# Kernel tuning notes

Hardware: AMD Instinct MI355X
Metric: run time of the kernel (lower is better)

The kernel has to match this reference:

```python
import math
import jax, jax.numpy as jnp
import numpy as np

D_MODEL = 1024
D_HIDDEN = 2048
N_EXPERTS = 8
TOP_K = 2
CAPACITY_FACTOR = 1.25


def setup_inputs() -> dict:
    key = jax.random.key(0)
    k0, k1, k2, k3 = jax.random.split(key, 4)
    B, T = 2, 2048
    x = jax.random.normal(k0, (B, T, D_MODEL), dtype=jnp.float32)
    # torch nn.Linear stores weight as [out_features, in_features]
    w_router = jax.random.normal(k1, (N_EXPERTS, D_MODEL), dtype=jnp.float32) * 0.02
    w_gate = jax.random.normal(k2, (D_HIDDEN, D_MODEL), dtype=jnp.float32) * 0.02
    w_down = jax.random.normal(k3, (N_EXPERTS, D_MODEL, D_HIDDEN), dtype=jnp.float32) * 0.02
    return {"x": x, "w_router": w_router, "w_gate": w_gate, "w_down": w_down}


def _moe_forward(x, w_router, w_gate, w_down):
    B, T, D = x.shape
    N = B * T
    xf = x.reshape(N, D)

    # Router (computed in fp32, as in the original)
    logits = xf.astype(jnp.float32) @ w_router.T            # [N, E]
    gates = jax.nn.softmax(logits, axis=-1)                  # [N, E]
    topk_gates, topk_idx = jax.lax.top_k(gates, TOP_K)       # [N, K]

    # expert_mask[n, e] = 1 if expert e is among token n's top-k
    expert_mask = jax.nn.one_hot(topk_idx, N_EXPERTS, dtype=jnp.int32).sum(axis=1)  # [N, E]

    # Capacity masking via cumulative position within each expert's buffer
    capacity = math.ceil(N / N_EXPERTS * CAPACITY_FACTOR)
    position_in_expert = jnp.cumsum(expert_mask, axis=0) - 1
    expert_mask = expert_mask * (position_in_expert < capacity)

    keep = jnp.take_along_axis(expert_mask, topk_idx, axis=1) > 0  # [N, K]
    topk_gates = topk_gates * keep
    topk_gates = topk_gates / (topk_gates.sum(axis=-1, keepdims=True) + 1e-6)

    # Shared up-projection + SiLU (dropout = 0)
    hidden = jax.nn.silu(xf @ w_gate.T)                      # [N, H]

    # combine[n, e] = sum_k topk_gates[n, k] * [topk_idx[n, k] == e]
    combine = (topk_gates[:, :, None]
               * jax.nn.one_hot(topk_idx, N_EXPERTS, dtype=topk_gates.dtype)).sum(axis=1)  # [N, E]

    # Combine: y[n] = sum_e combine[n, e] * (hidden[n] @ w_down[e].T)
    # (dropped tokens have combine weight 0, matching the gated index_add in torch)
    y = jnp.zeros((N, D), dtype=x.dtype)
    for e in range(N_EXPERTS):  # small fixed loop over experts
        y = y + combine[:, e:e + 1] * (hidden @ w_down[e].T)
    return y.reshape(B, T, D)


def reference(x, w_router, w_gate, w_down):
    return _moe_forward(x, w_router, w_gate, w_down)
```

## Files before the change

### kernel.cpp

```cpp
#include <hip/hip_runtime.h>
#include <hip/hip_bf16.h>
#include <math.h>

#define NTOK 4096
#define DMODEL 1024
#define DHID 2048
#define NEXP 8
#define CAP 640

typedef __attribute__((ext_vector_type(8))) short short8;
typedef __attribute__((ext_vector_type(4))) float f32x4;

__device__ inline short f2bf(float f) {
    union { float f; unsigned u; } v; v.f = f;
    unsigned r = v.u + 0x7FFF + ((v.u >> 16) & 1);
    return (short)(r >> 16);
}

__global__ __launch_bounds__(256) void router_kernel(
        const float* __restrict__ x, const float* __restrict__ wr,
        int2* __restrict__ topk_idx, float2* __restrict__ topk_gate)
{
    const int token = blockIdx.x * 4 + (threadIdx.x >> 6);
    const int lane  = threadIdx.x & 63;
    const float* xr = x + (size_t)token * DMODEL + lane * 16;
    float acc[NEXP];
#pragma unroll
    for (int e = 0; e < NEXP; e++) acc[e] = 0.f;
#pragma unroll
    for (int j = 0; j < 4; j++) {
        float4 xv = ((const float4*)xr)[j];
#pragma unroll
        for (int e = 0; e < NEXP; e++) {
            float4 wv = ((const float4*)(wr + e * DMODEL + lane * 16))[j];
            acc[e] += xv.x * wv.x + xv.y * wv.y + xv.z * wv.z + xv.w * wv.w;
        }
    }
#pragma unroll
    for (int off = 32; off >= 1; off >>= 1) {
#pragma unroll
        for (int e = 0; e < NEXP; e++) acc[e] += __shfl_xor(acc[e], off, 64);
    }
    if (lane == 0) {
        float m = acc[0];
#pragma unroll
        for (int e = 1; e < NEXP; e++) m = fmaxf(m, acc[e]);
        float den = 0.f, g[NEXP];
#pragma unroll
        for (int e = 0; e < NEXP; e++) { g[e] = __expf(acc[e] - m); den += g[e]; }
        float inv = 1.f / den;
#pragma unroll
        for (int e = 0; e < NEXP; e++) g[e] *= inv;
        int i0 = 0; float l0 = acc[0];
#pragma unroll
        for (int e = 1; e < NEXP; e++) if (acc[e] > l0) { l0 = acc[e]; i0 = e; }
        int i1 = -1; float l1 = -1e30f;
#pragma unroll
        for (int e = 0; e < NEXP; e++) if (e != i0 && acc[e] > l1) { l1 = acc[e]; i1 = e; }
        topk_idx[token]  = make_int2(i0, i1);
        topk_gate[token] = make_float2(g[i0], g[i1]);
    }
}

__global__ __launch_bounds__(1024) void scan_kernel(
        const int2* __restrict__ topk_idx, const float2* __restrict__ topk_gate,
        int* __restrict__ gtok, float* __restrict__ gw, int* __restrict__ gcnt)
{
    __shared__ unsigned long long sb0[1024], sb1[1024];
    const int th = threadIdx.x;
    int2 idx[4]; float2 gt[4];
#pragma unroll
    for (int j = 0; j < 4; j++) { idx[j] = topk_idx[th * 4 + j]; gt[j] = topk_gate[th * 4 + j]; }
    unsigned long long c0 = 0, c1 = 0;
#pragma unroll
    for (int j = 0; j < 4; j++) {
        int e0 = idx[j].x, e1 = idx[j].y;
        if (e0 < 4) c0 += 1ull << (e0 * 16); else c1 += 1ull << ((e0 - 4) * 16);
        if (e1 < 4) c0 += 1ull << (e1 * 16); else c1 += 1ull << ((e1 - 4) * 16);
    }
    const unsigned long long my0 = c0, my1 = c1;
    sb0[th] = c0; sb1[th] = c1;
    __syncthreads();
    for (int d = 1; d < 1024; d <<= 1) {
        unsigned long long a0 = 0, a1 = 0;
        if (th >= d) { a0 = sb0[th - d]; a1 = sb1[th - d]; }
        __syncthreads();
        c0 += a0; c1 += a1;
        sb0[th] = c0; sb1[th] = c1;
        __syncthreads();
    }
    if (th == 1023) {
#pragma unroll
        for (int e = 0; e < 4; e++) gcnt[e]     = min((int)((c0 >> (e * 16)) & 0xFFFF), CAP);
#pragma unroll
        for (int e = 0; e < 4; e++) gcnt[4 + e] = min((int)((c1 >> (e * 16)) & 0xFFFF), CAP);
    }
    const unsigned long long x0 = c0 - my0, x1 = c1 - my1;
    int base[NEXP];
#pragma unroll
    for (int e = 0; e < 4; e++) base[e]     = (int)((x0 >> (e * 16)) & 0xFFFF);
#pragma unroll
    for (int e = 0; e < 4; e++) base[4 + e] = (int)((x1 >> (e * 16)) & 0xFFFF);
#pragma unroll
    for (int j = 0; j < 4; j++) {
        const int n = th * 4 + j;
        const int e0 = idx[j].x, e1 = idx[j].y;
        const int p0 = base[e0]++;
        const int p1 = base[e1]++;
        const bool k0 = p0 < CAP, k1 = p1 < CAP;
        const float gg0 = k0 ? gt[j].x : 0.f, gg1 = k1 ? gt[j].y : 0.f;
        const float invs = 1.f / (gg0 + gg1 + 1e-6f);
        if (k0) { gtok[e0 * CAP + p0] = n; gw[e0 * CAP + p0] = gg0 * invs; }
        if (k1) { gtok[e1 * CAP + p1] = n; gw[e1 * CAP + p1] = gg1 * invs; }
    }
}

__global__ __launch_bounds__(256) void gemm1_kernel(
        const float* __restrict__ X, const float* __restrict__ WG, short* __restrict__ Hid)
{
    __shared__ short As[128][72];
    __shared__ short Bs[128][72];
    const int t = threadIdx.x;
    const int wave = t >> 6, lane = t & 63;
    const int m0 = blockIdx.y * 128, n0 = blockIdx.x * 128;
    const int wm = (wave >> 1) * 64, wn = (wave & 1) * 64;
    const int lm = lane & 15, lq = lane >> 4, lk = lq * 8;
    const int r0 = t >> 3, c8 = (t & 7) * 8;

    f32x4 acc[4][4];
#pragma unroll
    for (int a = 0; a < 4; a++)
#pragma unroll
        for (int b = 0; b < 4; b++) acc[a][b] = (f32x4)(0.f);

    for (int k0 = 0; k0 < DMODEL; k0 += 64) {
#pragma unroll
        for (int i = 0; i < 4; i++) {
            const int row = r0 + i * 32;
            const float* ga = X + (size_t)(m0 + row) * DMODEL + k0 + c8;
            float4 v0 = ((const float4*)ga)[0];
            float4 v1 = ((const float4*)ga)[1];
            short8 s = { f2bf(v0.x), f2bf(v0.y), f2bf(v0.z), f2bf(v0.w),
                         f2bf(v1.x), f2bf(v1.y), f2bf(v1.z), f2bf(v1.w) };
            *(short8*)&As[row][c8] = s;
            const float* gb = WG + (size_t)(n0 + row) * DMODEL + k0 + c8;
            float4 w0 = ((const float4*)gb)[0];
            float4 w1 = ((const float4*)gb)[1];
            short8 sw = { f2bf(w0.x), f2bf(w0.y), f2bf(w0.z), f2bf(w0.w),
                          f2bf(w1.x), f2bf(w1.y), f2bf(w1.z), f2bf(w1.w) };
            *(short8*)&Bs[row][c8] = sw;
        }
        __syncthreads();
#pragma unroll
        for (int kk = 0; kk < 64; kk += 32) {
            short8 af[4], bf[4];
#pragma unroll
            for (int mi = 0; mi < 4; mi++) af[mi] = *(const short8*)&As[wm + mi * 16 + lm][kk + lk];
#pragma unroll
            for (int ni = 0; ni < 4; ni++) bf[ni] = *(const short8*)&Bs[wn + ni * 16 + lm][kk + lk];
#pragma unroll
            for (int mi = 0; mi < 4; mi++)
#pragma unroll
                for (int ni = 0; ni < 4; ni++)
                    acc[mi][ni] = __builtin_amdgcn_mfma_f32_16x16x32_bf16(af[mi], bf[ni], acc[mi][ni], 0, 0, 0);
        }
        __syncthreads();
    }
#pragma unroll
    for (int mi = 0; mi < 4; mi++)
#pragma unroll
        for (int i = 0; i < 4; i++) {
            const int row = m0 + wm + mi * 16 + lq * 4 + i;
#pragma unroll
            for (int ni = 0; ni < 4; ni++) {
                const int col = n0 + wn + ni * 16 + lm;
                const float v = acc[mi][ni][i];
                const float s = v / (1.f + __expf(-v));
                Hid[(size_t)row * DHID + col] = f2bf(s);
            }
        }
}

__global__ __launch_bounds__(256) void gemm2_kernel(
        const short* __restrict__ Hid, const float* __restrict__ WD,
        const int* __restrict__ gtok, const float* __restrict__ gw,
        const int* __restrict__ gcnt, float* __restrict__ Y)
{
    __shared__ short As[128][72];
    __shared__ short Bs[128][72];
    __shared__ int   tok_s[128];
    __shared__ float w_s[128];
    const int e = blockIdx.z;
    const int cnt = gcnt[e];
    const int m0 = blockIdx.y * 128;
    if (m0 >= cnt) return;
    const int n0 = blockIdx.x * 128;
    const int t = threadIdx.x;
    const int wave = t >> 6, lane = t & 63;
    const int wm = (wave >> 1) * 64, wn = (wave & 1) * 64;
    const int lm = lane & 15, lq = lane >> 4, lk = lq * 8;
    const int r0 = t >> 3, c8 = (t & 7) * 8;
    const float* WDe = WD + (size_t)e * DMODEL * DHID;

    if (t < 128) {
        const int r = m0 + t;
        const bool v = r < cnt;
        tok_s[t] = v ? gtok[e * CAP + r] : 0;
        w_s[t]   = v ? gw[e * CAP + r] : 0.f;
    }
    __syncthreads();

    f32x4 acc[4][4];
#pragma unroll
    for (int a = 0; a < 4; a++)
#pragma unroll
        for (int b = 0; b < 4; b++) acc[a][b] = (f32x4)(0.f);

    const int tokA[4] = { tok_s[r0], tok_s[r0 + 32], tok_s[r0 + 64], tok_s[r0 + 96] };

    for (int k0 = 0; k0 < DHID; k0 += 64) {
#pragma unroll
        for (int i = 0; i < 4; i++) {
            const int row = r0 + i * 32;
            uint4 av = *(const uint4*)(Hid + (size_t)tokA[i] * DHID + k0 + c8);
            *(uint4*)&As[row][c8] = av;
            const float* gb = WDe + (size_t)(n0 + row) * DHID + k0 + c8;
            float4 w0 = ((const float4*)gb)[0];
            float4 w1 = ((const float4*)gb)[1];
            short8 sw = { f2bf(w0.x), f2bf(w0.y), f2bf(w0.z), f2bf(w0.w),
                          f2bf(w1.x), f2bf(w1.y), f2bf(w1.z), f2bf(w1.w) };
            *(short8*)&Bs[row][c8] = sw;
        }
        __syncthreads();
#pragma unroll
        for (int kk = 0; kk < 64; kk += 32) {
            short8 af[4], bf[4];
#pragma unroll
            for (int mi = 0; mi < 4; mi++) af[mi] = *(const short8*)&As[wm + mi * 16 + lm][kk + lk];
#pragma unroll
            for (int ni = 0; ni < 4; ni++) bf[ni] = *(const short8*)&Bs[wn + ni * 16 + lm][kk + lk];
#pragma unroll
            for (int mi = 0; mi < 4; mi++)
#pragma unroll
                for (int ni = 0; ni < 4; ni++)
                    acc[mi][ni] = __builtin_amdgcn_mfma_f32_16x16x32_bf16(af[mi], bf[ni], acc[mi][ni], 0, 0, 0);
        }
        __syncthreads();
    }
#pragma unroll
    for (int mi = 0; mi < 4; mi++)
#pragma unroll
        for (int i = 0; i < 4; i++) {
            const int r = wm + mi * 16 + lq * 4 + i;
            const float wr = w_s[r];
            if (wr > 0.f) {
                const int token = tok_s[r];
#pragma unroll
                for (int ni = 0; ni < 4; ni++) {
                    const int col = n0 + wn + ni * 16 + lm;
                    atomicAdd(&Y[(size_t)token * DMODEL + col], acc[mi][ni][i] * wr);
                }
            }
        }
}

extern "C" void kernel_launch(void* const* d_in, const int* in_sizes, int n_in,
                              void* d_out, int out_size, void* d_ws, size_t ws_size,
                              hipStream_t stream) {
    const float* x  = (const float*)d_in[0];
    const float* wr = (const float*)d_in[1];
    const float* wg = (const float*)d_in[2];
    const float* wd = (const float*)d_in[3];
    float* y = (float*)d_out;

    char* w = (char*)d_ws;
    int2*   topk_idx  = (int2*)w;    w += NTOK * sizeof(int2);
    float2* topk_gate = (float2*)w;  w += NTOK * sizeof(float2);
    int*    gtok      = (int*)w;     w += NEXP * CAP * sizeof(int);
    float*  gw        = (float*)w;   w += NEXP * CAP * sizeof(float);
    int*    gcnt      = (int*)w;     w += 256;
    short*  Hid       = (short*)w;   w += (size_t)NTOK * DHID * sizeof(short);

    hipMemsetAsync(y, 0, (size_t)NTOK * DMODEL * sizeof(float), stream);
    router_kernel<<<NTOK / 4, 256, 0, stream>>>(x, wr, topk_idx, topk_gate);
    scan_kernel<<<1, 1024, 0, stream>>>(topk_idx, topk_gate, gtok, gw, gcnt);
    gemm1_kernel<<<dim3(DHID / 128, NTOK / 128), 256, 0, stream>>>(x, wg, Hid);
    gemm2_kernel<<<dim3(DMODEL / 128, (CAP + 127) / 128, NEXP), 256, 0, stream>>>(Hid, wd, gtok, gw, gcnt, y);
}
```

Baseline: 251.3 us.

## Pre-convert operands to bf16 and stream GEMM tiles with async global-to-LDS loads

```diff
diff --git a/kernel.cpp b/kernel.cpp
--- a/kernel.cpp
+++ b/kernel.cpp
@@ -17,7 +17,68 @@
     return (short)(r >> 16);
 }
 
+__device__ inline void async16(const short* g, short* l) {
+    __builtin_amdgcn_global_load_lds(
+        (const __attribute__((address_space(1))) unsigned*)g,
+        (__attribute__((address_space(3))) unsigned*)l, 16, 0, 0);
+}
+
 __global__ __launch_bounds__(256) void router_kernel(
+        const float* __restrict__ x, const float* __restrict__ wr, short* __restrict__ Xb,
+        int2* __restrict__ topk_idx, float2* __restrict__ topk_gate)
+{
+    const int token = blockIdx.x * 4 + (threadIdx.x >> 6);
+    const int lane  = threadIdx.x & 63;
+    const float* xr = x + (size_t)token * DMODEL + lane * 16;
+    float4 xv[4];
+#pragma unroll
+    for (int j = 0; j < 4; j++) xv[j] = ((const float4*)xr)[j];
+    short8 s0 = { f2bf(xv[0].x), f2bf(xv[0].y), f2bf(xv[0].z), f2bf(xv[0].w),
+                  f2bf(xv[1].x), f2bf(xv[1].y), f2bf(xv[1].z), f2bf(xv[1].w) };
+    short8 s1 = { f2bf(xv[2].x), f2bf(xv[2].y), f2bf(xv[2].z), f2bf(xv[2].w),
+                  f2bf(xv[3].x), f2bf(xv[3].y), f2bf(xv[3].z), f2bf(xv[3].w) };
+    short* xo = Xb + (size_t)token * DMODEL + lane * 16;
+    *(short8*)xo = s0;
+    *(short8*)(xo + 8) = s1;
+
+    float acc[NEXP];
+#pragma unroll
+    for (int e = 0; e < NEXP; e++) acc[e] = 0.f;
+#pragma unroll
+    for (int j = 0; j < 4; j++) {
+#pragma unroll
+        for (int e = 0; e < NEXP; e++) {
+            float4 wv = ((const float4*)(wr + e * DMODEL + lane * 16))[j];
+            acc[e] += xv[j].x * wv.x + xv[j].y * wv.y + xv[j].z * wv.z + xv[j].w * wv.w;
+        }
+    }
+#pragma unroll
+    for (int off = 32; off >= 1; off >>= 1) {
+#pragma unroll
+        for (int e = 0; e < NEXP; e++) acc[e] += __shfl_xor(acc[e], off, 64);
+    }
+    if (lane == 0) {
+        float m = acc[0];
+#pragma unroll
+        for (int e = 1; e < NEXP; e++) m = fmaxf(m, acc[e]);
+        float den = 0.f, g[NEXP];
+#pragma unroll
+        for (int e = 0; e < NEXP; e++) { g[e] = __expf(acc[e] - m); den += g[e]; }
+        float inv = 1.f / den;
+#pragma unroll
+        for (int e = 0; e < NEXP; e++) g[e] *= inv;
+        int i0 = 0; float l0 = acc[0];
+#pragma unroll
+        for (int e = 1; e < NEXP; e++) if (acc[e] > l0) { l0 = acc[e]; i0 = e; }
+        int i1 = -1; float l1 = -1e30f;
+#pragma unroll
+        for (int e = 0; e < NEXP; e++) if (e != i0 && acc[e] > l1) { l1 = acc[e]; i1 = e; }
+        topk_idx[token]  = make_int2(i0, i1);
+        topk_gate[token] = make_float2(g[i0], g[i1]);
+    }
+}
+
+__global__ __launch_bounds__(256) void router_fb_kernel(
         const float* __restrict__ x, const float* __restrict__ wr,
         int2* __restrict__ topk_idx, float2* __restrict__ topk_gate)
 {
@@ -62,12 +123,23 @@
     }
 }
 
+__global__ __launch_bounds__(256) void convert_kernel(
+        const float* __restrict__ src, short* __restrict__ dst)
+{
+    const size_t base = ((size_t)blockIdx.x * 256 + threadIdx.x) * 8;
+    float4 a = ((const float4*)(src + base))[0];
+    float4 b = ((const float4*)(src + base))[1];
+    short8 s = { f2bf(a.x), f2bf(a.y), f2bf(a.z), f2bf(a.w),
+                 f2bf(b.x), f2bf(b.y), f2bf(b.z), f2bf(b.w) };
+    *(short8*)(dst + base) = s;
+}
+
 __global__ __launch_bounds__(1024) void scan_kernel(
         const int2* __restrict__ topk_idx, const float2* __restrict__ topk_gate,
         int* __restrict__ gtok, float* __restrict__ gw, int* __restrict__ gcnt)
 {
-    __shared__ unsigned long long sb0[1024], sb1[1024];
-    const int th = threadIdx.x;
+    __shared__ unsigned long long wt0[16], wt1[16];
+    const int th = threadIdx.x, lane = th & 63, wid = th >> 6;
     int2 idx[4]; float2 gt[4];
 #pragma unroll
     for (int j = 0; j < 4; j++) { idx[j] = topk_idx[th * 4 + j]; gt[j] = topk_gate[th * 4 + j]; }
@@ -79,16 +151,17 @@
         if (e1 < 4) c0 += 1ull << (e1 * 16); else c1 += 1ull << ((e1 - 4) * 16);
     }
     const unsigned long long my0 = c0, my1 = c1;
-    sb0[th] = c0; sb1[th] = c1;
+#pragma unroll
+    for (int d = 1; d < 64; d <<= 1) {
+        unsigned long long t0 = __shfl_up(c0, d, 64);
+        unsigned long long t1 = __shfl_up(c1, d, 64);
+        if (lane >= d) { c0 += t0; c1 += t1; }
+    }
+    if (lane == 63) { wt0[wid] = c0; wt1[wid] = c1; }
     __syncthreads();
-    for (int d = 1; d < 1024; d <<= 1) {
-        unsigned long long a0 = 0, a1 = 0;
-        if (th >= d) { a0 = sb0[th - d]; a1 = sb1[th - d]; }
-        __syncthreads();
-        c0 += a0; c1 += a1;
-        sb0[th] = c0; sb1[th] = c1;
-        __syncthreads();
-    }
+    unsigned long long o0 = 0, o1 = 0;
+    for (int w = 0; w < wid; w++) { o0 += wt0[w]; o1 += wt1[w]; }
+    c0 += o0; c1 += o1;
     if (th == 1023) {
 #pragma unroll
         for (int e = 0; e < 4; e++) gcnt[e]     = min((int)((c0 >> (e * 16)) & 0xFFFF), CAP);
@@ -116,6 +189,149 @@
 }
 
 __global__ __launch_bounds__(256) void gemm1_kernel(
+        const short* __restrict__ Xb, const short* __restrict__ WGb, short* __restrict__ Hid)
+{
+    __shared__ __align__(16) short As[128 * 64];
+    __shared__ __align__(16) short Bs[128 * 64];
+    const int t = threadIdx.x;
+    const int wave = t >> 6, lane = t & 63;
+    const int m0 = blockIdx.y * 128, n0 = blockIdx.x * 128;
+    const int wm = (wave >> 1) * 64, wn = (wave & 1) * 64;
+    const int lm = lane & 15, lq = lane >> 4, lk = lq * 8;
+
+    const short *ga[4], *gb[4];
+    short *la[4], *lb[4];
+#pragma unroll
+    for (int j = 0; j < 4; j++) {
+        const int c = j * 256 + t, r = c >> 3, col = (c & 7) * 8;
+        la[j] = &As[c * 8]; lb[j] = &Bs[c * 8];
+        ga[j] = Xb  + (size_t)(m0 + r) * DMODEL + col;
+        gb[j] = WGb + (size_t)(n0 + r) * DMODEL + col;
+    }
+
+    f32x4 acc[4][4];
+#pragma unroll
+    for (int a = 0; a < 4; a++)
+#pragma unroll
+        for (int b = 0; b < 4; b++) acc[a][b] = (f32x4)(0.f);
+
+    for (int k0 = 0; k0 < DMODEL; k0 += 64) {
+#pragma unroll
+        for (int j = 0; j < 4; j++) { async16(ga[j] + k0, la[j]); async16(gb[j] + k0, lb[j]); }
+        __syncthreads();
+#pragma unroll
+        for (int kk = 0; kk < 64; kk += 32) {
+            short8 af[4], bf[4];
+#pragma unroll
+            for (int mi = 0; mi < 4; mi++) af[mi] = *(const short8*)&As[(wm + mi * 16 + lm) * 64 + kk + lk];
+#pragma unroll
+            for (int ni = 0; ni < 4; ni++) bf[ni] = *(const short8*)&Bs[(wn + ni * 16 + lm) * 64 + kk + lk];
+#pragma unroll
+            for (int mi = 0; mi < 4; mi++)
+#pragma unroll
+                for (int ni = 0; ni < 4; ni++)
+                    acc[mi][ni] = __builtin_amdgcn_mfma_f32_16x16x32_bf16(af[mi], bf[ni], acc[mi][ni], 0, 0, 0);
+        }
+        __syncthreads();
+    }
+#pragma unroll
+    for (int mi = 0; mi < 4; mi++)
+#pragma unroll
+        for (int i = 0; i < 4; i++) {
+            const int row = m0 + wm + mi * 16 + lq * 4 + i;
+#pragma unroll
+            for (int ni = 0; ni < 4; ni++) {
+                const int col = n0 + wn + ni * 16 + lm;
+                const float v = acc[mi][ni][i];
+                const float s = v / (1.f + __expf(-v));
+                Hid[(size_t)row * DHID + col] = f2bf(s);
+            }
+        }
+}
+
+__global__ __launch_bounds__(256) void gemm2_kernel(
+        const short* __restrict__ Hid, const short* __restrict__ WDb,
+        const int* __restrict__ gtok, const float* __restrict__ gw,
+        const int* __restrict__ gcnt, float* __restrict__ Y)
+{
+    __shared__ __align__(16) short As[128 * 64];
+    __shared__ __align__(16) short Bs[128 * 64];
+    __shared__ int   tok_s[128];
+    __shared__ float w_s[128];
+    const int e  = blockIdx.x;
+    const int n0 = blockIdx.y * 128;
+    const int m0 = (blockIdx.z >> 1) * 128;
+    const int ks = blockIdx.z & 1;
+    const int cnt = gcnt[e];
+    if (m0 >= cnt) return;
+    const int t = threadIdx.x;
+    const int wave = t >> 6, lane = t & 63;
+    const int wm = (wave >> 1) * 64, wn = (wave & 1) * 64;
+    const int lm = lane & 15, lq = lane >> 4, lk = lq * 8;
+    const short* WDe = WDb + (size_t)e * DMODEL * DHID;
+
+    if (t < 128) {
+        const int r = m0 + t;
+        const bool v = r < cnt;
+        tok_s[t] = v ? gtok[e * CAP + r] : 0;
+        w_s[t]   = v ? gw[e * CAP + r] : 0.f;
+    }
+    __syncthreads();
+
+    const short *ga[4], *gb[4];
+    short *la[4], *lb[4];
+#pragma unroll
+    for (int j = 0; j < 4; j++) {
+        const int c = j * 256 + t, r = c >> 3, col = (c & 7) * 8;
+        la[j] = &As[c * 8]; lb[j] = &Bs[c * 8];
+        ga[j] = Hid + (size_t)tok_s[r] * DHID + col;
+        gb[j] = WDe + (size_t)(n0 + r) * DHID + col;
+    }
+
+    f32x4 acc[4][4];
+#pragma unroll
+    for (int a = 0; a < 4; a++)
+#pragma unroll
+        for (int b = 0; b < 4; b++) acc[a][b] = (f32x4)(0.f);
+
+    const int kbeg = ks * (DHID / 2), kend = kbeg + DHID / 2;
+    for (int k0 = kbeg; k0 < kend; k0 += 64) {
+#pragma unroll
+        for (int j = 0; j < 4; j++) { async16(ga[j] + k0, la[j]); async16(gb[j] + k0, lb[j]); }
+        __syncthreads();
+#pragma unroll
+        for (int kk = 0; kk < 64; kk += 32) {
+            short8 af[4], bf[4];
+#pragma unroll
+            for (int mi = 0; mi < 4; mi++) af[mi] = *(const short8*)&As[(wm + mi * 16 + lm) * 64 + kk + lk];
+#pragma unroll
+            for (int ni = 0; ni < 4; ni++) bf[ni] = *(const short8*)&Bs[(wn + ni * 16 + lm) * 64 + kk + lk];
+#pragma unroll
+            for (int mi = 0; mi < 4; mi++)
+#pragma unroll
+                for (int ni = 0; ni < 4; ni++)
+                    acc[mi][ni] = __builtin_amdgcn_mfma_f32_16x16x32_bf16(af[mi], bf[ni], acc[mi][ni], 0, 0, 0);
+        }
+        __syncthreads();
+    }
+#pragma unroll
+    for (int mi = 0; mi < 4; mi++)
+#pragma unroll
+        for (int i = 0; i < 4; i++) {
+            const int r = wm + mi * 16 + lq * 4 + i;
+            const float wr = w_s[r];
+            if (wr > 0.f) {
+                const int token = tok_s[r];
+#pragma unroll
+                for (int ni = 0; ni < 4; ni++) {
+                    const int col = n0 + wn + ni * 16 + lm;
+                    atomicAdd(&Y[(size_t)token * DMODEL + col], acc[mi][ni][i] * wr);
+                }
+            }
+        }
+}
+
+__global__ __launch_bounds__(256) void gemm1_fb_kernel(
         const float* __restrict__ X, const float* __restrict__ WG, short* __restrict__ Hid)
 {
     __shared__ short As[128][72];
@@ -181,7 +397,7 @@
         }
 }
 
-__global__ __launch_bounds__(256) void gemm2_kernel(
+__global__ __launch_bounds__(256) void gemm2_fb_kernel(
         const short* __restrict__ Hid, const float* __restrict__ WD,
         const int* __restrict__ gtok, const float* __restrict__ gw,
         const int* __restrict__ gcnt, float* __restrict__ Y)
@@ -280,10 +496,26 @@
     float*  gw        = (float*)w;   w += NEXP * CAP * sizeof(float);
     int*    gcnt      = (int*)w;     w += 256;
     short*  Hid       = (short*)w;   w += (size_t)NTOK * DHID * sizeof(short);
+    short*  Xb        = (short*)w;   w += (size_t)NTOK * DMODEL * sizeof(short);
+    short*  WGb       = (short*)w;   w += (size_t)DHID * DMODEL * sizeof(short);
+    short*  WDb       = (short*)w;   w += (size_t)NEXP * DMODEL * DHID * sizeof(short);
+    const size_t need_full = (size_t)(w - (char*)d_ws);
 
     hipMemsetAsync(y, 0, (size_t)NTOK * DMODEL * sizeof(float), stream);
-    router_kernel<<<NTOK / 4, 256, 0, stream>>>(x, wr, topk_idx, topk_gate);
-    scan_kernel<<<1, 1024, 0, stream>>>(topk_idx, topk_gate, gtok, gw, gcnt);
-    gemm1_kernel<<<dim3(DHID / 128, NTOK / 128), 256, 0, stream>>>(x, wg, Hid);
-    gemm2_kernel<<<dim3(DMODEL / 128, (CAP + 127) / 128, NEXP), 256, 0, stream>>>(Hid, wd, gtok, gw, gcnt, y);
-}
+
+    if (ws_size >= need_full) {
+        router_kernel<<<NTOK / 4, 256, 0, stream>>>(x, wr, Xb, topk_idx, topk_gate);
+        convert_kernel<<<(DHID * DMODEL) / (256 * 8), 256, 0, stream>>>(wg, WGb);
+        convert_kernel<<<(NEXP * DMODEL * DHID) / (256 * 8), 256, 0, stream>>>(wd, WDb);
+        scan_kernel<<<1, 1024, 0, stream>>>(topk_idx, topk_gate, gtok, gw, gcnt);
+        gemm1_kernel<<<dim3(DHID / 128, NTOK / 128), 256, 0, stream>>>(Xb, WGb, Hid);
+        gemm2_kernel<<<dim3(NEXP, DMODEL / 128, 2 * ((CAP + 127) / 128)), 256, 0, stream>>>(
+            Hid, WDb, gtok, gw, gcnt, y);
+    } else {
+        router_fb_kernel<<<NTOK / 4, 256, 0, stream>>>(x, wr, topk_idx, topk_gate);
+        scan_kernel<<<1, 1024, 0, stream>>>(topk_idx, topk_gate, gtok, gw, gcnt);
+        gemm1_fb_kernel<<<dim3(DHID / 128, NTOK / 128), 256, 0, stream>>>(x, wg, Hid);
+        gemm2_fb_kernel<<<dim3(DMODEL / 128, (CAP + 127) / 128, NEXP), 256, 0, stream>>>(
+            Hid, wd, gtok, gw, gcnt, y);
+    }
+}
```

New measurement: 248.9 us. About the same (-0.9%).
